# Performance work log

Hardware: AMD Instinct MI355X
Metric: run time of the kernel (lower is better)

The kernel has to match this reference:

```python
import jax, jax.numpy as jnp
import numpy as np

N = 100000
E = 1600000
D_IN = 64
D_HID = 64
D_OUT = 40
BN_EPS = 1e-5


def setup_inputs() -> dict:
    key = jax.random.key(0)
    ks = jax.random.split(key, 8)
    x = jax.random.normal(ks[0], (N, D_IN), dtype=jnp.float32)
    edge_index = jax.random.randint(ks[1], (2, E), 0, N, dtype=jnp.int64)
    # SAGEConv params: out = lin_l(aggr_neigh) + lin_r(x); bias lives in lin_l
    s1 = 1.0 / np.sqrt(D_IN)
    W1l = jax.random.uniform(ks[2], (D_HID, D_IN), jnp.float32, -s1, s1)
    W1r = jax.random.uniform(ks[3], (D_HID, D_IN), jnp.float32, -s1, s1)
    b1 = jnp.zeros((D_HID,), jnp.float32)
    gamma = jnp.ones((D_HID,), jnp.float32)
    beta = jnp.zeros((D_HID,), jnp.float32)
    s2 = 1.0 / np.sqrt(D_HID)
    W2l = jax.random.uniform(ks[4], (D_OUT, D_HID), jnp.float32, -s2, s2)
    W2r = jax.random.uniform(ks[5], (D_OUT, D_HID), jnp.float32, -s2, s2)
    b2 = jnp.zeros((D_OUT,), jnp.float32)
    return {"x": x, "edge_index": edge_index, "W1l": W1l, "W1r": W1r, "b1": b1,
            "gamma": gamma, "beta": beta, "W2l": W2l, "W2r": W2r, "b2": b2}


def _scatter_mean(feat, src, dst, n):
    # gather source-node features, scatter-mean onto destination nodes
    summed = jax.ops.segment_sum(feat[src], dst, num_segments=n)  # [N, D]
    cnt = jax.ops.segment_sum(jnp.ones((src.shape[0],), feat.dtype), dst, num_segments=n)
    return summed / jnp.maximum(cnt, 1.0)[:, None]


def _sage_conv(h, src, dst, Wl, Wr, b):
    agg = _scatter_mean(h, src, dst, h.shape[0])
    return agg @ Wl.T + h @ Wr.T + b


def reference(x, edge_index, W1l, W1r, b1, gamma, beta, W2l, W2r, b2):
    src, dst = edge_index[0], edge_index[1]
    h = _sage_conv(x, src, dst, W1l, W1r, b1)
    # BatchNorm1d (training-mode batch statistics, biased variance)
    mu = jnp.mean(h, axis=0)
    var = jnp.mean(jnp.square(h - mu), axis=0)
    h = (h - mu) * jax.lax.rsqrt(var + BN_EPS) * gamma + beta
    h = jax.nn.relu(h)
    # dropout is identity in eval mode
    out = _sage_conv(h, src, dst, W2l, W2r, b2)
    return out
```

## Files before the change

### kernel.cpp

```cpp
#include <hip/hip_runtime.h>
#include <hip/hip_fp8.h>

#define N_NODES 100000
#define N_EDGES 1600000
#define BN_EPS 1e-5f
#define E4 400000
#define CAP 64
#define NBINS 391
#define BINCAP 4608
#define BIN_MASK 255
#define G_BLOCKS 6250
#define NCOPY 32
#define D1B 391

typedef float v2f __attribute__((ext_vector_type(2)));
typedef __attribute__((ext_vector_type(8))) short bf16x8;
typedef __attribute__((ext_vector_type(4))) float f32x4;

__device__ __forceinline__ float bcast(float v, int k) {
    return __uint_as_float(__builtin_amdgcn_readlane(__float_as_uint(v), k));
}
__device__ __forceinline__ unsigned short f2bf(float x) {
    unsigned int u = __float_as_uint(x);
    return (unsigned short)((u + 0x7FFF + ((u >> 16) & 1)) >> 16);
}
__device__ __forceinline__ bf16x8 pack8(float4 a, float4 b) {
    bf16x8 r;
    r[0] = (short)f2bf(a.x); r[1] = (short)f2bf(a.y);
    r[2] = (short)f2bf(a.z); r[3] = (short)f2bf(a.w);
    r[4] = (short)f2bf(b.x); r[5] = (short)f2bf(b.y);
    r[6] = (short)f2bf(b.z); r[7] = (short)f2bf(b.w);
    return r;
}
__device__ __forceinline__ unsigned char f2fp8(float x) {
    return (unsigned char)__hip_cvt_float_to_fp8(x, __HIP_SATFINITE, __HIP_E4M3);
}
template <bool HI>
__device__ __forceinline__ v2f fp8x2(unsigned int w) {
#if __has_builtin(__builtin_amdgcn_cvt_pk_f32_fp8)
    return __builtin_amdgcn_cvt_pk_f32_fp8((int)w, HI);
#else
    unsigned int b = HI ? (w >> 16) : w;
    __half_raw h0 = __hip_cvt_fp8_to_halfraw((__hip_fp8_storage_t)(b & 0xFF), __HIP_E4M3);
    __half_raw h1 = __hip_cvt_fp8_to_halfraw((__hip_fp8_storage_t)((b >> 8) & 0xFF), __HIP_E4M3);
    v2f r; r.x = __half2float(__half(h0)); r.y = __half2float(__half(h1));
    return r;
#endif
}

__global__ __launch_bounds__(1024) void binA_kernel(
    const int4* __restrict__ src4, const int4* __restrict__ dst4,
    int* __restrict__ bcur, unsigned int* __restrict__ binbuf)
{
    __shared__ int lcnt[NBINS];
    __shared__ int lbase[NBINS];
    int tid = threadIdx.x;
    if (tid < NBINS) lcnt[tid] = 0;
    __syncthreads();

    int i = blockIdx.x * 1024 + tid;
    int4 d, s;
    int b0 = 0, b1 = 0, b2 = 0, b3 = 0, r0 = 0, r1 = 0, r2 = 0, r3 = 0;
    bool valid = (i < E4);
    if (valid) {
        d = dst4[i]; s = src4[i];
        b0 = d.x >> 8; r0 = atomicAdd(&lcnt[b0], 1);
        b1 = d.y >> 8; r1 = atomicAdd(&lcnt[b1], 1);
        b2 = d.z >> 8; r2 = atomicAdd(&lcnt[b2], 1);
        b3 = d.w >> 8; r3 = atomicAdd(&lcnt[b3], 1);
    }
    __syncthreads();
    if (tid < NBINS && lcnt[tid] > 0)
        lbase[tid] = atomicAdd(&bcur[tid], lcnt[tid]);
    __syncthreads();
    if (valid) {
        int p;
        p = lbase[b0] + r0; if (p < BINCAP) binbuf[(size_t)b0 * BINCAP + p] = ((unsigned)s.x << 8) | (unsigned)(d.x & BIN_MASK);
        p = lbase[b1] + r1; if (p < BINCAP) binbuf[(size_t)b1 * BINCAP + p] = ((unsigned)s.y << 8) | (unsigned)(d.y & BIN_MASK);
        p = lbase[b2] + r2; if (p < BINCAP) binbuf[(size_t)b2 * BINCAP + p] = ((unsigned)s.z << 8) | (unsigned)(d.z & BIN_MASK);
        p = lbase[b3] + r3; if (p < BINCAP) binbuf[(size_t)b3 * BINCAP + p] = ((unsigned)s.w << 8) | (unsigned)(d.w & BIN_MASK);
    }
}

__global__ __launch_bounds__(256) void binB_dense1_kernel(
    const unsigned int* __restrict__ binbuf, const int* __restrict__ bcur,
    int* __restrict__ cnt, int* __restrict__ nbrf,
    const float* __restrict__ x, const float* __restrict__ W1l,
    const float* __restrict__ W1r, const float* __restrict__ b1,
    unsigned char* __restrict__ u8, float* __restrict__ hv)
{
    if (blockIdx.x < NBINS) {
        __shared__ int lc[256];
        int tid = threadIdx.x;
        lc[tid] = 0;
        __syncthreads();
        int bin = blockIdx.x;
        int n = min(bcur[bin], BINCAP);
        for (int i = tid; i < n; i += 256) {
            unsigned int e = binbuf[(size_t)bin * BINCAP + i];
            int dl  = (int)(e & BIN_MASK);
            int src = (int)(e >> 8);
            int slot = atomicAdd(&lc[dl], 1);
            if (slot < CAP)
                nbrf[((size_t)(bin * 256 + dl)) * CAP + slot] = src;
        }
        __syncthreads();
        int node = bin * 256 + tid;
        if (node < N_NODES) {
            int c = min(lc[tid], CAP);
            cnt[node] = c;
            if (c == 0) nbrf[(size_t)node * CAP] = 0;
        }
        return;
    }

    int lane = threadIdx.x & 63;
    int wv   = threadIdx.x >> 6;
    int lr   = lane & 15;
    int lk   = lane >> 4;

    bf16x8 Bf[2][4][2];
#pragma unroll
    for (int mat = 0; mat < 2; ++mat) {
        const float* W = mat ? W1r : W1l;
#pragma unroll
        for (int ft = 0; ft < 4; ++ft) {
#pragma unroll
            for (int kh = 0; kh < 2; ++kh) {
                const float* p = W + (size_t)(ft * 16 + lr) * 64 + kh * 32 + lk * 8;
                Bf[mat][ft][kh] = pack8(*(const float4*)p, *(const float4*)(p + 4));
            }
        }
    }
    float b1v[4];
#pragma unroll
    for (int ft = 0; ft < 4; ++ft) b1v[ft] = b1[ft * 16 + lr];

    int nb = (blockIdx.x - NBINS) * 256;

    for (int it = 0; it < 4; ++it) {
        int n0 = nb + it * 64 + wv * 16;
        int arow = min(n0 + lr, N_NODES - 1);
        const float* xp = x + (size_t)arow * 64 + lk * 8;
        bf16x8 a0 = pack8(*(const float4*)xp,        *(const float4*)(xp + 4));
        bf16x8 a1 = pack8(*(const float4*)(xp + 32), *(const float4*)(xp + 36));

#pragma unroll
        for (int ft = 0; ft < 4; ++ft) {
            f32x4 Cl = {0.f, 0.f, 0.f, 0.f};
            f32x4 Cr = {0.f, 0.f, 0.f, 0.f};
            Cl = __builtin_amdgcn_mfma_f32_16x16x32_bf16(a0, Bf[0][ft][0], Cl, 0, 0, 0);
            Cl = __builtin_amdgcn_mfma_f32_16x16x32_bf16(a1, Bf[0][ft][1], Cl, 0, 0, 0);
            Cr = __builtin_amdgcn_mfma_f32_16x16x32_bf16(a0, Bf[1][ft][0], Cr, 0, 0, 0);
            Cr = __builtin_amdgcn_mfma_f32_16x16x32_bf16(a1, Bf[1][ft][1], Cr, 0, 0, 0);
#pragma unroll
            for (int r = 0; r < 4; ++r) {
                int node = n0 + lk * 4 + r;
                if (node < N_NODES) {
                    u8[(size_t)node * 64 + ft * 16 + lr] = f2fp8(Cl[r]);
                    hv[(size_t)node * 64 + ft * 16 + lr] = Cr[r] + b1v[ft];
                }
            }
        }
    }
}

__global__ __launch_bounds__(256) void gather1_bn_kernel(
    const unsigned short* __restrict__ u16, const int* __restrict__ cnt,
    const int* __restrict__ nbrf, float* __restrict__ hv,
    float* __restrict__ sumsR)
{
    __shared__ int sdeg[16];
    int node0 = blockIdx.x * 16;
    if (threadIdx.x < 16) {
        int n = node0 + threadIdx.x;
        sdeg[threadIdx.x] = (n < N_NODES) ? min(cnt[n], CAP) : 0;
    }
    __syncthreads();

    int lane = threadIdx.x & 63;
    int m    = lane & 31;
    int half = lane >> 5;
    int wv   = threadIdx.x >> 6;
    float s1_0 = 0.f, s1_1 = 0.f, s2_0 = 0.f, s2_1 = 0.f;

    int d0  = sdeg[wv];
    int idn = nbrf[(size_t)min(node0 + wv, N_NODES - 1) * CAP + min(lane, max(d0, 1) - 1)];

    for (int nn = 0; nn < 4; ++nn) {
        int li   = nn * 4 + wv;
        int node = node0 + li;
        int deg  = sdeg[li];
        int id   = idn;

        if (nn < 3) {
            int lin = li + 4;
            int dn  = sdeg[lin];
            idn = nbrf[(size_t)min(node0 + lin, N_NODES - 1) * CAP + min(lane, max(dn, 1) - 1)];
        }

        if (node < N_NODES) {
            float2 v = make_float2(0.f, 0.f);
            if (half == 0)
                v = ((const float2*)hv)[(size_t)node * 32 + m];

            float p0=0,p1=0,p2=0,p3=0,q0=0,q1=0,q2=0,q3=0;
            for (int r = 0; r < deg; r += 16) {
#pragma unroll
                for (int i = 0; i < 8; ++i) {
                    int e   = r + 2 * i + half;
                    int ide = __shfl(id, e);
                    unsigned int w = u16[(size_t)ide * 32 + m];
                    w = (e < deg) ? w : 0u;
                    v2f d = fp8x2<false>(w);
                    if ((i & 3) == 0)      { p0 += d.x; q0 += d.y; }
                    else if ((i & 3) == 1) { p1 += d.x; q1 += d.y; }
                    else if ((i & 3) == 2) { p2 += d.x; q2 += d.y; }
                    else                   { p3 += d.x; q3 += d.y; }
                }
            }
            float P = (p0 + p1) + (p2 + p3);
            float Q = (q0 + q1) + (q2 + q3);
            P += __shfl_xor(P, 32);
            Q += __shfl_xor(Q, 32);
            if (half == 0) {
                float inv = 1.0f / (float)max(deg, 1);
                float h0 = P * inv + v.x;
                float h1 = Q * inv + v.y;
                ((float2*)hv)[(size_t)node * 32 + m] = make_float2(h0, h1);
                s1_0 += h0; s1_1 += h1;
                s2_0 += h0 * h0; s2_1 += h1 * h1;
            }
        }
    }

    __shared__ float2 redA[256];
    __shared__ float2 redB[256];
    redA[threadIdx.x] = make_float2(s1_0, s1_1);
    redB[threadIdx.x] = make_float2(s2_0, s2_1);
    __syncthreads();
    if (threadIdx.x < 32) {
        int mm = threadIdx.x;
        float a0=0,a1=0,b0=0,b1=0;
        for (int w = 0; w < 4; ++w) {
            float2 A = redA[w * 64 + mm]; a0 += A.x; a1 += A.y;
            float2 B = redB[w * 64 + mm]; b0 += B.x; b1 += B.y;
        }
        float* base = sumsR + (size_t)(blockIdx.x & (NCOPY - 1)) * 128;
        atomicAdd(&base[2 * mm], a0);       atomicAdd(&base[2 * mm + 1], a1);
        atomicAdd(&base[64 + 2 * mm], b0);  atomicAdd(&base[64 + 2 * mm + 1], b1);
    }
}

__global__ __launch_bounds__(256) void dense2_bn_kernel(
    const float* __restrict__ h, const float* __restrict__ sumsR,
    const float* __restrict__ gamma, const float* __restrict__ beta,
    const float* __restrict__ W2l, const float* __restrict__ W2r,
    const float* __restrict__ b2,
    unsigned char* __restrict__ t40, float* __restrict__ out)
{
    __shared__ float ssc[64];
    __shared__ float ssh[64];
    if (threadIdx.x < 64) {
        int f = threadIdx.x;
        float s = 0.f, q = 0.f;
#pragma unroll
        for (int c = 0; c < NCOPY; ++c) {
            s += sumsR[c * 128 + f];
            q += sumsR[c * 128 + 64 + f];
        }
        float inv_n = 1.0f / (float)N_NODES;
        float mu  = s * inv_n;
        float var = q * inv_n - mu * mu;
        float rs  = rsqrtf(var + BN_EPS);
        float sc  = gamma[f] * rs;
        ssc[f] = sc;
        ssh[f] = beta[f] - mu * sc;
    }
    __syncthreads();

    int lane = threadIdx.x & 63;
    int wv   = threadIdx.x >> 6;
    int lr   = lane & 15;
    int lk   = lane >> 4;

    float scA[8], shA[8], scB[8], shB[8];
#pragma unroll
    for (int j = 0; j < 8; ++j) {
        scA[j] = ssc[lk * 8 + j];      shA[j] = ssh[lk * 8 + j];
        scB[j] = ssc[32 + lk * 8 + j]; shB[j] = ssh[32 + lk * 8 + j];
    }

    bf16x8 Bt[3][2], Bo[3][2];
#pragma unroll
    for (int ft = 0; ft < 3; ++ft) {
        int row = min(ft * 16 + lr, 39);
#pragma unroll
        for (int kh = 0; kh < 2; ++kh) {
            const float* pl = W2l + (size_t)row * 64 + kh * 32 + lk * 8;
            const float* pr = W2r + (size_t)row * 64 + kh * 32 + lk * 8;
            Bt[ft][kh] = pack8(*(const float4*)pl, *(const float4*)(pl + 4));
            Bo[ft][kh] = pack8(*(const float4*)pr, *(const float4*)(pr + 4));
        }
    }
    float b2v[3];
#pragma unroll
    for (int ft = 0; ft < 3; ++ft) b2v[ft] = b2[min(ft * 16 + lr, 39)];

    int nb = blockIdx.x * 256;

    for (int it = 0; it < 4; ++it) {
        int n0 = nb + it * 64 + wv * 16;
        int arow = min(n0 + lr, N_NODES - 1);
        const float* hp = h + (size_t)arow * 64 + lk * 8;
        float4 h0a = *(const float4*)hp,        h0b = *(const float4*)(hp + 4);
        float4 h1a = *(const float4*)(hp + 32), h1b = *(const float4*)(hp + 36);
        float4 n0a, n0b, n1a, n1b;
        n0a.x = fmaxf(h0a.x * scA[0] + shA[0], 0.f);
        n0a.y = fmaxf(h0a.y * scA[1] + shA[1], 0.f);
        n0a.z = fmaxf(h0a.z * scA[2] + shA[2], 0.f);
        n0a.w = fmaxf(h0a.w * scA[3] + shA[3], 0.f);
        n0b.x = fmaxf(h0b.x * scA[4] + shA[4], 0.f);
        n0b.y = fmaxf(h0b.y * scA[5] + shA[5], 0.f);
        n0b.z = fmaxf(h0b.z * scA[6] + shA[6], 0.f);
        n0b.w = fmaxf(h0b.w * scA[7] + shA[7], 0.f);
        n1a.x = fmaxf(h1a.x * scB[0] + shB[0], 0.f);
        n1a.y = fmaxf(h1a.y * scB[1] + shB[1], 0.f);
        n1a.z = fmaxf(h1a.z * scB[2] + shB[2], 0.f);
        n1a.w = fmaxf(h1a.w * scB[3] + shB[3], 0.f);
        n1b.x = fmaxf(h1b.x * scB[4] + shB[4], 0.f);
        n1b.y = fmaxf(h1b.y * scB[5] + shB[5], 0.f);
        n1b.z = fmaxf(h1b.z * scB[6] + shB[6], 0.f);
        n1b.w = fmaxf(h1b.w * scB[7] + shB[7], 0.f);
        bf16x8 a0 = pack8(n0a, n0b);
        bf16x8 a1 = pack8(n1a, n1b);

#pragma unroll
        for (int ft = 0; ft < 3; ++ft) {
            f32x4 Ct = {0.f, 0.f, 0.f, 0.f};
            f32x4 Co = {0.f, 0.f, 0.f, 0.f};
            Ct = __builtin_amdgcn_mfma_f32_16x16x32_bf16(a0, Bt[ft][0], Ct, 0, 0, 0);
            Ct = __builtin_amdgcn_mfma_f32_16x16x32_bf16(a1, Bt[ft][1], Ct, 0, 0, 0);
            Co = __builtin_amdgcn_mfma_f32_16x16x32_bf16(a0, Bo[ft][0], Co, 0, 0, 0);
            Co = __builtin_amdgcn_mfma_f32_16x16x32_bf16(a1, Bo[ft][1], Co, 0, 0, 0);
            int f = ft * 16 + lr;
#pragma unroll
            for (int r = 0; r < 4; ++r) {
                int node = n0 + lk * 4 + r;
                if (node < N_NODES && f < 40) {
                    t40[(size_t)node * 64 + f] = f2fp8(Ct[r]);
                    out[(size_t)node * 40 + f] = Co[r] + b2v[ft];
                }
            }
        }
    }
}

__global__ __launch_bounds__(256) void gather2_kernel(
    const unsigned int* __restrict__ t40, const int* __restrict__ cnt,
    const int* __restrict__ nbrf, float* __restrict__ out)
{
    __shared__ int sdeg[16];
    int node0 = blockIdx.x * 16;
    if (threadIdx.x < 16) {
        int n = node0 + threadIdx.x;
        sdeg[threadIdx.x] = (n < N_NODES) ? min(cnt[n], CAP) : 0;
    }
    __syncthreads();

    int lane = threadIdx.x & 63;
    int q    = lane >> 4;
    int m    = lane & 15;
    int cl   = (m < 10) ? m : 9;
    int wv   = threadIdx.x >> 6;

    int dA = sdeg[wv], dB = sdeg[wv + 4];
    int idA = nbrf[(size_t)min(node0 + wv,     N_NODES - 1) * CAP + min(lane, max(dA, 1) - 1)];
    int idB = nbrf[(size_t)min(node0 + wv + 4, N_NODES - 1) * CAP + min(lane, max(dB, 1) - 1)];

    unsigned int r0A[4], r1A[4], r0B[4], r1B[4];
    {
        int cnt0 = dA;
#pragma unroll
        for (int i = 0; i < 4; ++i) {
            int e   = 4 * i + q;
            int ide = __shfl(idA, max(min(e, cnt0 - 1), 0));
            r0A[i] = t40[(size_t)ide * 16 + cl];
        }
        if (cnt0 > 16) {
#pragma unroll
            for (int i = 0; i < 4; ++i) {
                int e   = 16 + 4 * i + q;
                int ide = __shfl(idA, min(e, cnt0 - 1));
                r1A[i] = t40[(size_t)ide * 16 + cl];
            }
        }
    }

    for (int nn = 0; nn < 4; ++nn) {
        int li   = nn * 4 + wv;
        int node = node0 + li;
        int deg  = sdeg[li];

        int idC = 0;
        if (nn < 2) {
            int lic = li + 8;
            int dc  = sdeg[lic];
            idC = nbrf[(size_t)min(node0 + lic, N_NODES - 1) * CAP + min(lane, max(dc, 1) - 1)];
        }
        if (nn < 3) {
            int cntn = sdeg[li + 4];
#pragma unroll
            for (int i = 0; i < 4; ++i) {
                int e   = 4 * i + q;
                int ide = __shfl(idB, max(min(e, cntn - 1), 0));
                r0B[i] = t40[(size_t)ide * 16 + cl];
            }
            if (cntn > 16) {
#pragma unroll
                for (int i = 0; i < 4; ++i) {
                    int e   = 16 + 4 * i + q;
                    int ide = __shfl(idB, min(e, cntn - 1));
                    r1B[i] = t40[(size_t)ide * 16 + cl];
                }
            }
        }

        if (node < N_NODES) {
            float4 o = make_float4(0.f, 0.f, 0.f, 0.f);
            if (lane < 10)
                o = ((const float4*)out)[(size_t)node * 10 + m];

            float a0=0,a1=0,a2=0,a3=0, b0=0,b1=0,b2=0,b3=0;
#pragma unroll
            for (int i = 0; i < 4; ++i) {
                int e = 4 * i + q;
                unsigned int w = (e < deg) ? r0A[i] : 0u;
                v2f dlo = fp8x2<false>(w);
                v2f dhi = fp8x2<true>(w);
                if (i & 1) { b0 += dlo.x; b1 += dlo.y; b2 += dhi.x; b3 += dhi.y; }
                else       { a0 += dlo.x; a1 += dlo.y; a2 += dhi.x; a3 += dhi.y; }
            }
            if (deg > 16) {
#pragma unroll
                for (int i = 0; i < 4; ++i) {
                    int e = 16 + 4 * i + q;
                    unsigned int w = (e < deg) ? r1A[i] : 0u;
                    v2f dlo = fp8x2<false>(w);
                    v2f dhi = fp8x2<true>(w);
                    if (i & 1) { b0 += dlo.x; b1 += dlo.y; b2 += dhi.x; b3 += dhi.y; }
                    else       { a0 += dlo.x; a1 += dlo.y; a2 += dhi.x; a3 += dhi.y; }
                }
                for (int r = 32; r < deg; r += 16) {
#pragma unroll
                    for (int i = 0; i < 4; ++i) {
                        int e   = r + 4 * i + q;
                        int ide = __shfl(idA, min(e, deg - 1));
                        unsigned int w = t40[(size_t)ide * 16 + cl];
                        w = (e < deg) ? w : 0u;
                        v2f dlo = fp8x2<false>(w);
                        v2f dhi = fp8x2<true>(w);
                        if (i & 1) { b0 += dlo.x; b1 += dlo.y; b2 += dhi.x; b3 += dhi.y; }
                        else       { a0 += dlo.x; a1 += dlo.y; a2 += dhi.x; a3 += dhi.y; }
                    }
                }
            }
            a0 += b0; a1 += b1; a2 += b2; a3 += b3;
            a0 += __shfl_xor(a0, 16); a0 += __shfl_xor(a0, 32);
            a1 += __shfl_xor(a1, 16); a1 += __shfl_xor(a1, 32);
            a2 += __shfl_xor(a2, 16); a2 += __shfl_xor(a2, 32);
            a3 += __shfl_xor(a3, 16); a3 += __shfl_xor(a3, 32);
            if (lane < 10) {
                float inv = 1.0f / (float)max(deg, 1);
                o.x += a0 * inv;
                o.y += a1 * inv;
                o.z += a2 * inv;
                o.w += a3 * inv;
                ((float4*)out)[(size_t)node * 10 + m] = o;
            }
        }

        idA = idB; idB = idC;
#pragma unroll
        for (int i = 0; i < 4; ++i) { r0A[i] = r0B[i]; r1A[i] = r1B[i]; }
    }
}

extern "C" void kernel_launch(void* const* d_in, const int* in_sizes, int n_in,
                              void* d_out, int out_size, void* d_ws, size_t ws_size,
                              hipStream_t stream)
{
    const float* x     = (const float*)d_in[0];
    const int*   ei    = (const int*)d_in[1];
    const float* W1l   = (const float*)d_in[2];
    const float* W1r   = (const float*)d_in[3];
    const float* b1    = (const float*)d_in[4];
    const float* gamma = (const float*)d_in[5];
    const float* beta  = (const float*)d_in[6];
    const float* W2l   = (const float*)d_in[7];
    const float* W2r   = (const float*)d_in[8];
    const float* b2    = (const float*)d_in[9];
    float* out = (float*)d_out;

    const int4* src4 = (const int4*)ei;
    const int4* dst4 = (const int4*)(ei + N_EDGES);

    float* ws    = (float*)d_ws;
    float* hv    = ws;
    float* sumsR = hv + (size_t)N_NODES * 64;
    int* bcur = (int*)(sumsR + NCOPY * 128);
    int* cnt  = bcur + 392;
    int* nbrf = cnt + N_NODES;
    unsigned char* u8 = (unsigned char*)(nbrf + (size_t)N_NODES * 64);
    unsigned char* t40 = u8;
    unsigned int* binbuf = (unsigned int*)d_out;

    dim3 blk(256);

    (void)hipMemsetAsync(sumsR, 0, (size_t)(NCOPY * 128 + 392) * 4, stream);

    binA_kernel<<<391, 1024, 0, stream>>>(src4, dst4, bcur, binbuf);

    binB_dense1_kernel<<<NBINS + D1B, blk, 0, stream>>>(
        binbuf, bcur, cnt, nbrf, x, W1l, W1r, b1, u8, hv);

    gather1_bn_kernel<<<G_BLOCKS, blk, 0, stream>>>(
        (const unsigned short*)u8, cnt, nbrf, hv, sumsR);

    dense2_bn_kernel<<<D1B, blk, 0, stream>>>(
        hv, sumsR, gamma, beta, W2l, W2r, b2, t40, out);
    gather2_kernel<<<G_BLOCKS, blk, 0, stream>>>(
        (const unsigned int*)t40, cnt, nbrf, out);
}
```

Before: 225.2 us.

## Stage per-node neighbor lists in LDS and write CSR rows coalesced

The bin-to-CSR pass now runs with 1024-thread blocks. It reads bin entries as uint4 and first collects each node's neighbors into a shared-memory bucket. Afterwards it writes full 64-entry neighbor rows with int4 stores, replacing the scattered per-edge global writes. The fused dense1 path is regrouped to 1024 nodes per block so the shared launch size still fits. Per-node capacity drops from 64 to 62 slots, and the large static LDS allocation limits occupancy for both branches.

```diff
diff --git a/kernel.cpp b/kernel.cpp
--- a/kernel.cpp
+++ b/kernel.cpp
@@ -6,20 +6,19 @@
 #define BN_EPS 1e-5f
 #define E4 400000
 #define CAP 64
+#define SLOTS 62
 #define NBINS 391
 #define BINCAP 4608
 #define BIN_MASK 255
 #define G_BLOCKS 6250
 #define NCOPY 32
-#define D1B 391
+#define D1B 98
+#define D2B 391
 
 typedef float v2f __attribute__((ext_vector_type(2)));
 typedef __attribute__((ext_vector_type(8))) short bf16x8;
 typedef __attribute__((ext_vector_type(4))) float f32x4;
 
-__device__ __forceinline__ float bcast(float v, int k) {
-    return __uint_as_float(__builtin_amdgcn_readlane(__float_as_uint(v), k));
-}
 __device__ __forceinline__ unsigned short f2bf(float x) {
     unsigned int u = __float_as_uint(x);
     return (unsigned short)((u + 0x7FFF + ((u >> 16) & 1)) >> 16);
@@ -82,40 +81,67 @@
     }
 }
 
-__global__ __launch_bounds__(256) void binB_dense1_kernel(
+__global__ __launch_bounds__(1024) void binB_dense1_kernel(
     const unsigned int* __restrict__ binbuf, const int* __restrict__ bcur,
     int* __restrict__ cnt, int* __restrict__ nbrf,
     const float* __restrict__ x, const float* __restrict__ W1l,
     const float* __restrict__ W1r, const float* __restrict__ b1,
     unsigned char* __restrict__ u8, float* __restrict__ hv)
 {
+    __shared__ int bucket[256][SLOTS];
+    __shared__ int lc[256];
+
+    int tid = threadIdx.x;
+
     if (blockIdx.x < NBINS) {
-        __shared__ int lc[256];
-        int tid = threadIdx.x;
-        lc[tid] = 0;
+        if (tid < 256) lc[tid] = 0;
         __syncthreads();
         int bin = blockIdx.x;
         int n = min(bcur[bin], BINCAP);
-        for (int i = tid; i < n; i += 256) {
-            unsigned int e = binbuf[(size_t)bin * BINCAP + i];
-            int dl  = (int)(e & BIN_MASK);
-            int src = (int)(e >> 8);
-            int slot = atomicAdd(&lc[dl], 1);
-            if (slot < CAP)
-                nbrf[((size_t)(bin * 256 + dl)) * CAP + slot] = src;
+        const uint4* bb = (const uint4*)(binbuf + (size_t)bin * BINCAP);
+        int n4 = (n + 3) >> 2;
+        for (int i = tid; i < n4; i += 1024) {
+            uint4 e4 = bb[i];
+            int base = i * 4;
+#pragma unroll
+            for (int k = 0; k < 4; ++k) {
+                unsigned int e = (k == 0) ? e4.x : (k == 1) ? e4.y : (k == 2) ? e4.z : e4.w;
+                if (base + k < n) {
+                    int dl = (int)(e & BIN_MASK);
+                    int slot = atomicAdd(&lc[dl], 1);
+                    if (slot < SLOTS) bucket[dl][slot] = (int)(e >> 8);
+                }
+            }
         }
         __syncthreads();
-        int node = bin * 256 + tid;
-        if (node < N_NODES) {
-            int c = min(lc[tid], CAP);
-            cnt[node] = c;
-            if (c == 0) nbrf[(size_t)node * CAP] = 0;
+        if (tid < 256) {
+            int node = bin * 256 + tid;
+            if (node < N_NODES) cnt[node] = min(lc[tid], SLOTS);
+            if (lc[tid] == 0) bucket[tid][0] = 0;
+        }
+        __syncthreads();
+        {
+            int node = tid >> 2, q = tid & 3;
+            int gnode = bin * 256 + node;
+            if (gnode < N_NODES) {
+                int* dst = nbrf + (size_t)gnode * CAP + q * 16;
+#pragma unroll
+                for (int j4 = 0; j4 < 4; ++j4) {
+                    int s = q * 16 + j4 * 4;
+                    int4 v;
+                    v.x = (s + 0 < SLOTS) ? bucket[node][s + 0] : 0;
+                    v.y = (s + 1 < SLOTS) ? bucket[node][s + 1] : 0;
+                    v.z = (s + 2 < SLOTS) ? bucket[node][s + 2] : 0;
+                    v.w = (s + 3 < SLOTS) ? bucket[node][s + 3] : 0;
+                    *(int4*)(dst + j4 * 4) = v;
+                }
+            }
         }
         return;
     }
 
-    int lane = threadIdx.x & 63;
-    int wv   = threadIdx.x >> 6;
+    int lane = tid & 63;
+    int wv   = tid >> 6;
     int lr   = lane & 15;
     int lk   = lane >> 4;
 
@@ -136,10 +162,11 @@
 #pragma unroll
     for (int ft = 0; ft < 4; ++ft) b1v[ft] = b1[ft * 16 + lr];
 
-    int nb = (blockIdx.x - NBINS) * 256;
+    int nb = (blockIdx.x - NBINS) * 1024;
 
     for (int it = 0; it < 4; ++it) {
-        int n0 = nb + it * 64 + wv * 16;
+        int n0 = nb + it * 256 + wv * 16;
+        if (n0 >= N_NODES) break;
         int arow = min(n0 + lr, N_NODES - 1);
         const float* xp = x + (size_t)arow * 64 + lk * 8;
         bf16x8 a0 = pack8(*(const float4*)xp,        *(const float4*)(xp + 4));
@@ -313,8 +340,9 @@
         int n0 = nb + it * 64 + wv * 16;
         int arow = min(n0 + lr, N_NODES - 1);
         const float* hp = h + (size_t)arow * 64 + lk * 8;
-        float4 h0a = *(const float4*)hp,        h0b = *(const float4*)(hp + 4);
+        float4 h0a = *(const float4*)hp,        float4_h0b = *(const float4*)(hp + 4);
         float4 h1a = *(const float4*)(hp + 32), h1b = *(const float4*)(hp + 36);
+        float4 h0b = float4_h0b;
         float4 n0a, n0b, n1a, n1b;
         n0a.x = fmaxf(h0a.x * scA[0] + shA[0], 0.f);
         n0a.y = fmaxf(h0a.y * scA[1] + shA[1], 0.f);
@@ -515,20 +543,18 @@
     unsigned char* t40 = u8;
     unsigned int* binbuf = (unsigned int*)d_out;
 
-    dim3 blk(256);
-
     (void)hipMemsetAsync(sumsR, 0, (size_t)(NCOPY * 128 + 392) * 4, stream);
 
     binA_kernel<<<391, 1024, 0, stream>>>(src4, dst4, bcur, binbuf);
 
-    binB_dense1_kernel<<<NBINS + D1B, blk, 0, stream>>>(
+    binB_dense1_kernel<<<NBINS + D1B, 1024, 0, stream>>>(
         binbuf, bcur, cnt, nbrf, x, W1l, W1r, b1, u8, hv);
 
-    gather1_bn_kernel<<<G_BLOCKS, blk, 0, stream>>>(
+    gather1_bn_kernel<<<G_BLOCKS, 256, 0, stream>>>(
         (const unsigned short*)u8, cnt, nbrf, hv, sumsR);
 
-    dense2_bn_kernel<<<D1B, blk, 0, stream>>>(
+    dense2_bn_kernel<<<D2B, 256, 0, stream>>>(
         hv, sumsR, gamma, beta, W2l, W2r, b2, t40, out);
-    gather2_kernel<<<G_BLOCKS, blk, 0, stream>>>(
+    gather2_kernel<<<G_BLOCKS, 256, 0, stream>>>(
         (const unsigned int*)t40, cnt, nbrf, out);
 }
```

Result: slower. 255.8 us (+13.6%).

## Replace fixed-capacity padded neighbor lists with compact CSR per-bin layout

Applied to the files above, without the earlier changes.

The per-bin neighbor build now counts degrees, does a shared-memory prefix scan, and writes neighbors contiguously into a compact CSR array with per-node offsets, instead of a padded N×64 table. The gather kernels read neighbor ids through those offsets. This cuts the neighbor-table footprint and the scattered writes into a 25.6 MB padded buffer, at the cost of an extra pass over each bin and a scan. Node-range guards were removed in the gathers, which relies on the workspace padding after offs and on G_BLOCKS*16 matching N exactly.

```diff
diff --git a/kernel.cpp b/kernel.cpp
--- a/kernel.cpp
+++ b/kernel.cpp
@@ -5,7 +5,6 @@
 #define N_EDGES 1600000
 #define BN_EPS 1e-5f
 #define E4 400000
-#define CAP 64
 #define NBINS 391
 #define BINCAP 4608
 #define BIN_MASK 255
@@ -17,9 +16,6 @@
 typedef __attribute__((ext_vector_type(8))) short bf16x8;
 typedef __attribute__((ext_vector_type(4))) float f32x4;
 
-__device__ __forceinline__ float bcast(float v, int k) {
-    return __uint_as_float(__builtin_amdgcn_readlane(__float_as_uint(v), k));
-}
 __device__ __forceinline__ unsigned short f2bf(float x) {
     unsigned int u = __float_as_uint(x);
     return (unsigned short)((u + 0x7FFF + ((u >> 16) & 1)) >> 16);
@@ -84,33 +80,50 @@
 
 __global__ __launch_bounds__(256) void binB_dense1_kernel(
     const unsigned int* __restrict__ binbuf, const int* __restrict__ bcur,
-    int* __restrict__ cnt, int* __restrict__ nbrf,
+    int* __restrict__ cnt, int* __restrict__ offs, int* __restrict__ nbrc,
     const float* __restrict__ x, const float* __restrict__ W1l,
     const float* __restrict__ W1r, const float* __restrict__ b1,
     unsigned char* __restrict__ u8, float* __restrict__ hv)
 {
     if (blockIdx.x < NBINS) {
         __shared__ int lc[256];
+        __shared__ int scan[256];
+        __shared__ int sexcl[256];
+        __shared__ int lc2[256];
         int tid = threadIdx.x;
-        lc[tid] = 0;
+        lc[tid] = 0; lc2[tid] = 0;
         __syncthreads();
-        int bin = blockIdx.x;
+        int bin  = blockIdx.x;
+        int binC = bin * BINCAP;
         int n = min(bcur[bin], BINCAP);
+        for (int i = tid; i < n; i += 256)
+            atomicAdd(&lc[binbuf[(size_t)bin * BINCAP + i] & BIN_MASK], 1);
+        __syncthreads();
+        scan[tid] = lc[tid];
+        __syncthreads();
+        for (int off = 1; off < 256; off <<= 1) {
+            int t = (tid >= off) ? scan[tid - off] : 0;
+            __syncthreads();
+            scan[tid] += t;
+            __syncthreads();
+        }
+        int excl = scan[tid] - lc[tid];
+        sexcl[tid] = excl;
+        int node = bin * 256 + tid;
+        if (node < N_NODES) {
+            offs[node] = binC + excl;
+            cnt[node]  = lc[tid];
+        }
+        __syncthreads();
         for (int i = tid; i < n; i += 256) {
             unsigned int e = binbuf[(size_t)bin * BINCAP + i];
-            int dl  = (int)(e & BIN_MASK);
-            int src = (int)(e >> 8);
-            int slot = atomicAdd(&lc[dl], 1);
-            if (slot < CAP)
-                nbrf[((size_t)(bin * 256 + dl)) * CAP + slot] = src;
-        }
-        __syncthreads();
-        int node = bin * 256 + tid;
-        if (node < N_NODES) {
-            int c = min(lc[tid], CAP);
-            cnt[node] = c;
-            if (c == 0) nbrf[(size_t)node * CAP] = 0;
-        }
+            int dl = (int)(e & BIN_MASK);
+            int slot = atomicAdd(&lc2[dl], 1);
+            nbrc[binC + sexcl[dl] + slot] = (int)(e >> 8);
+        }
+        int total = scan[255];
+        for (int t = tid; t < 64; t += 256)
+            if (total + t < BINCAP) nbrc[binC + total + t] = 0;
         return;
     }
 
@@ -167,14 +180,16 @@
 
 __global__ __launch_bounds__(256) void gather1_bn_kernel(
     const unsigned short* __restrict__ u16, const int* __restrict__ cnt,
-    const int* __restrict__ nbrf, float* __restrict__ hv,
-    float* __restrict__ sumsR)
+    const int* __restrict__ offs, const int* __restrict__ nbrc,
+    float* __restrict__ hv, float* __restrict__ sumsR)
 {
     __shared__ int sdeg[16];
+    __shared__ int soff[16];
     int node0 = blockIdx.x * 16;
     if (threadIdx.x < 16) {
         int n = node0 + threadIdx.x;
-        sdeg[threadIdx.x] = (n < N_NODES) ? min(cnt[n], CAP) : 0;
+        sdeg[threadIdx.x] = min(cnt[n], 64);
+        soff[threadIdx.x] = offs[n];
     }
     __syncthreads();
 
@@ -185,7 +200,7 @@
     float s1_0 = 0.f, s1_1 = 0.f, s2_0 = 0.f, s2_1 = 0.f;
 
     int d0  = sdeg[wv];
-    int idn = nbrf[(size_t)min(node0 + wv, N_NODES - 1) * CAP + min(lane, max(d0, 1) - 1)];
+    int idn = nbrc[soff[wv] + min(lane, max(d0, 1) - 1)];
 
     for (int nn = 0; nn < 4; ++nn) {
         int li   = nn * 4 + wv;
@@ -196,10 +211,10 @@
         if (nn < 3) {
             int lin = li + 4;
             int dn  = sdeg[lin];
-            idn = nbrf[(size_t)min(node0 + lin, N_NODES - 1) * CAP + min(lane, max(dn, 1) - 1)];
-        }
-
-        if (node < N_NODES) {
+            idn = nbrc[soff[lin] + min(lane, max(dn, 1) - 1)];
+        }
+
+        {
             float2 v = make_float2(0.f, 0.f);
             if (half == 0)
                 v = ((const float2*)hv)[(size_t)node * 32 + m];
@@ -358,13 +373,16 @@
 
 __global__ __launch_bounds__(256) void gather2_kernel(
     const unsigned int* __restrict__ t40, const int* __restrict__ cnt,
-    const int* __restrict__ nbrf, float* __restrict__ out)
+    const int* __restrict__ offs, const int* __restrict__ nbrc,
+    float* __restrict__ out)
 {
     __shared__ int sdeg[16];
+    __shared__ int soff[16];
     int node0 = blockIdx.x * 16;
     if (threadIdx.x < 16) {
         int n = node0 + threadIdx.x;
-        sdeg[threadIdx.x] = (n < N_NODES) ? min(cnt[n], CAP) : 0;
+        sdeg[threadIdx.x] = min(cnt[n], 64);
+        soff[threadIdx.x] = offs[n];
     }
     __syncthreads();
 
@@ -375,8 +393,8 @@
     int wv   = threadIdx.x >> 6;
 
     int dA = sdeg[wv], dB = sdeg[wv + 4];
-    int idA = nbrf[(size_t)min(node0 + wv,     N_NODES - 1) * CAP + min(lane, max(dA, 1) - 1)];
-    int idB = nbrf[(size_t)min(node0 + wv + 4, N_NODES - 1) * CAP + min(lane, max(dB, 1) - 1)];
+    int idA = nbrc[soff[wv]     + min(lane, max(dA, 1) - 1)];
+    int idB = nbrc[soff[wv + 4] + min(lane, max(dB, 1) - 1)];
 
     unsigned int r0A[4], r1A[4], r0B[4], r1B[4];
     {
@@ -406,7 +424,7 @@
         if (nn < 2) {
             int lic = li + 8;
             int dc  = sdeg[lic];
-            idC = nbrf[(size_t)min(node0 + lic, N_NODES - 1) * CAP + min(lane, max(dc, 1) - 1)];
+            idC = nbrc[soff[lic] + min(lane, max(dc, 1) - 1)];
         }
         if (nn < 3) {
             int cntn = sdeg[li + 4];
@@ -426,7 +444,7 @@
             }
         }
 
-        if (node < N_NODES) {
+        {
             float4 o = make_float4(0.f, 0.f, 0.f, 0.f);
             if (lane < 10)
                 o = ((const float4*)out)[(size_t)node * 10 + m];
@@ -510,25 +528,24 @@
     float* sumsR = hv + (size_t)N_NODES * 64;
     int* bcur = (int*)(sumsR + NCOPY * 128);
     int* cnt  = bcur + 392;
-    int* nbrf = cnt + N_NODES;
-    unsigned char* u8 = (unsigned char*)(nbrf + (size_t)N_NODES * 64);
+    int* offs = cnt + N_NODES;
+    int* nbrc = offs + N_NODES + 16;
+    unsigned char* u8 = (unsigned char*)(nbrc + (size_t)NBINS * BINCAP);
     unsigned char* t40 = u8;
     unsigned int* binbuf = (unsigned int*)d_out;
 
-    dim3 blk(256);
-
     (void)hipMemsetAsync(sumsR, 0, (size_t)(NCOPY * 128 + 392) * 4, stream);
 
     binA_kernel<<<391, 1024, 0, stream>>>(src4, dst4, bcur, binbuf);
 
-    binB_dense1_kernel<<<NBINS + D1B, blk, 0, stream>>>(
-        binbuf, bcur, cnt, nbrf, x, W1l, W1r, b1, u8, hv);
-
-    gather1_bn_kernel<<<G_BLOCKS, blk, 0, stream>>>(
-        (const unsigned short*)u8, cnt, nbrf, hv, sumsR);
-
-    dense2_bn_kernel<<<D1B, blk, 0, stream>>>(
+    binB_dense1_kernel<<<NBINS + D1B, 256, 0, stream>>>(
+        binbuf, bcur, cnt, offs, nbrc, x, W1l, W1r, b1, u8, hv);
+
+    gather1_bn_kernel<<<G_BLOCKS, 256, 0, stream>>>(
+        (const unsigned short*)u8, cnt, offs, nbrc, hv, sumsR);
+
+    dense2_bn_kernel<<<D1B, 256, 0, stream>>>(
         hv, sumsR, gamma, beta, W2l, W2r, b2, t40, out);
-    gather2_kernel<<<G_BLOCKS, blk, 0, stream>>>(
-        (const unsigned int*)t40, cnt, nbrf, out);
-}
+    gather2_kernel<<<G_BLOCKS, 256, 0, stream>>>(
+        (const unsigned int*)t40, cnt, offs, nbrc, out);
+}
```

Result: faster. 219.0 us (-2.7%).
